# Kernel optimization log

Hardware: AMD Instinct MI355X
Metric: run time of the kernel (lower is better)

The kernel has to match this reference:

```python
import jax, jax.numpy as jnp
import numpy as np

H = 16          # n_heads
HID = 64        # QASS MLP hidden dim


def setup_inputs() -> dict:
    key = jax.random.key(0)
    ks = jax.random.split(key, 12)
    B, N, D = 2, 2048, 1024
    Dh = D // H
    inp = {
        "query": jax.random.normal(ks[0], (B, N, D), jnp.float32),
        "key": jax.random.normal(ks[1], (B, N, D), jnp.float32),
        "value": jax.random.normal(ks[2], (B, N, D), jnp.float32),
        "allowed_mask": jnp.ones((1, 1, N, N), dtype=bool),
        # projection weights, torch Linear convention: y = x @ W.T, W: [out, in]
        "wq": jax.random.normal(ks[3], (D, D), jnp.float32) * (D ** -0.5),
        "wk": jax.random.normal(ks[4], (D, D), jnp.float32) * (D ** -0.5),
        "wv": jax.random.normal(ks[5], (D, D), jnp.float32) * (D ** -0.5),
        "wo": jax.random.normal(ks[6], (D, D), jnp.float32) * (D ** -0.5),
        # QASS scaler weights
        "wb1": jax.random.normal(ks[7], (HID, 1), jnp.float32),          # mlp_base[0]
        "wb2": jax.random.normal(ks[8], (H * Dh, HID), jnp.float32) * (HID ** -0.5),  # mlp_base[2]
        "wg1": jax.random.normal(ks[9], (HID, Dh), jnp.float32) * (Dh ** -0.5),       # mlp_gate[0]
        "wg2": jax.random.normal(ks[10], (Dh, HID), jnp.float32) * (HID ** -0.5),     # mlp_gate[2]
        "n_context": 2048,
    }
    return inp


def _gelu(x):
    return jax.nn.gelu(x, approximate=False)  # torch nn.GELU default (erf)


def reference(query, key, value, allowed_mask, wq, wk, wv, wo, wb1, wb2, wg1, wg2, n_context):
    B, N, D = query.shape
    Dh = D // H

    def split_heads(x):  # [B,N,D] -> [B,H,N,Dh]
        return x.reshape(B, N, H, Dh).transpose(0, 2, 1, 3)

    q = split_heads(query @ wq.T)
    k = split_heads(key @ wk.T)
    v = split_heads(value @ wv.T)

    # QASS scaling: q * base(log n) * (1 + tanh(gate(q)))   (n_context > 1)
    log_n = jnp.log(jnp.asarray(n_context, jnp.float32))
    base = (_gelu(log_n * wb1[:, 0]) @ wb2.T).reshape(1, H, 1, Dh)  # [1,H,1,Dh]
    gate = 1.0 + jnp.tanh(_gelu(q @ wg1.T) @ wg2.T)                  # [B,H,N,Dh]
    q = q * base * gate

    scores = jnp.einsum("bhnd,bhmd->bhnm", q, k) / jnp.sqrt(jnp.float32(Dh))
    scores = jnp.where(allowed_mask, scores, -jnp.inf)
    attn = jax.nn.softmax(scores, axis=-1)  # dropout p=0 -> identity
    out = jnp.einsum("bhnm,bhmd->bhnd", attn, v)
    out = out.transpose(0, 2, 1, 3).reshape(B, N, D)
    return out @ wo.T
```

## Files before the change

### kernel.cpp

```cpp
#include <hip/hip_runtime.h>
#include <math.h>


typedef _Float16 half_t;
using half8   = __attribute__((ext_vector_type(8))) _Float16;
using bhalf8  = __attribute__((ext_vector_type(8))) short;
using floatx4 = __attribute__((ext_vector_type(4))) float;

__device__ inline unsigned short f2bf(float f) {
  union { float f; unsigned int u; } v; v.f = f;
  unsigned int u = v.u;
  u = u + 0x7fffu + ((u >> 16) & 1u);
  return (unsigned short)(u >> 16);
}
__device__ inline float bf2f(unsigned short h) {
  union { unsigned int u; float f; } v; v.u = ((unsigned int)h) << 16;
  return v.f;
}
__device__ inline float gelu_f(float x) {
  return 0.5f * x * (1.0f + erff(x * 0.70710678118654752440f));
}
__device__ __forceinline__ unsigned int cvtpk_bf16(float lo, float hi) {
  unsigned int r;
  asm("v_cvt_pk_bf16_f32 %0, %1, %2" : "=v"(r) : "v"(lo), "v"(hi));
  return r;
}

#define MFMAF16(a, b, c)  __builtin_amdgcn_mfma_f32_16x16x32_f16((a), (b), (c), 0, 0, 0)
#define MFMABF16(a, b, c) __builtin_amdgcn_mfma_f32_16x16x32_bf16((a), (b), (c), 0, 0, 0)

__device__ __forceinline__ void dma16(const void* g, void* l) {
  __builtin_amdgcn_global_load_lds(
      (const __attribute__((address_space(1))) unsigned int*)g,
      (__attribute__((address_space(3))) unsigned int*)l, 16, 0, 0);
}

__global__ __launch_bounds__(256) void k_cvtbase(
    const float* __restrict__ q, const float* __restrict__ k, const float* __restrict__ v,
    const float* __restrict__ wq, const float* __restrict__ wk,
    const float* __restrict__ wv, const float* __restrict__ wo,
    half_t* __restrict__ q16, half_t* __restrict__ k16, half_t* __restrict__ v16,
    half_t* __restrict__ w16,
    const float* __restrict__ wb1, const float* __restrict__ wb2,
    const int* __restrict__ nctx, float* __restrict__ base_out) {
  int tid = threadIdx.x;
  if (blockIdx.x >= 8192) {
    __shared__ float h1[64];
    float logn = logf((float)(*nctx));
    if (tid < 64) h1[tid] = gelu_f(logn * wb1[tid]);
    __syncthreads();
    int i = (blockIdx.x - 8192) * 256 + tid;
    float s = 0.f;
#pragma unroll
    for (int j = 0; j < 64; j++) s += h1[j] * wb2[i * 64 + j];
    base_out[i] = s;
    return;
  }
  size_t e = ((size_t)blockIdx.x * 256 + tid) * 8;
  const float* src; half_t* dst; size_t off;
  if (e < (size_t)3 * 4194304) {
    int t = (int)(e >> 22); off = e & 4194303;
    src = (t == 0) ? q : (t == 1 ? k : v);
    dst = (t == 0) ? q16 : (t == 1 ? k16 : v16);
  } else {
    size_t e2 = e - (size_t)3 * 4194304;
    int t = (int)(e2 >> 20); off = (e2 & 1048575);
    src = (t == 0) ? wq : (t == 1 ? wk : (t == 2 ? wv : wo));
    dst = w16 + (size_t)t * 1048576;
  }
  float4 a = *(const float4*)(src + off);
  float4 b = *(const float4*)(src + off + 4);
  half8 h;
  h[0] = (half_t)a.x; h[1] = (half_t)a.y; h[2] = (half_t)a.z; h[3] = (half_t)a.w;
  h[4] = (half_t)b.x; h[5] = (half_t)b.y; h[6] = (half_t)b.z; h[7] = (half_t)b.w;
  *(half8*)(dst + off) = h;
}

template <int MODE>
__global__ __launch_bounds__(256, 3) void k_gemm(const half_t* __restrict__ Abase,
                                                 const half_t* __restrict__ Wbase,
                                                 half_t* __restrict__ qp16,
                                                 half_t* __restrict__ kswz,
                                                 unsigned short* __restrict__ vtl,
                                                 float* __restrict__ outf) {
  const int z = (MODE == 0) ? blockIdx.z : 0;
  const half_t* Ag = Abase + (size_t)z * 4194304;
  const half_t* Wg = Wbase + (size_t)z * 1048576;
  __shared__ __align__(16) half_t SM[2][128 * 64];
  half_t* As = SM[0];
  half_t* Bs = SM[1];
  const int tid = threadIdx.x, lane = tid & 63, w = tid >> 6;
  const int quad = lane >> 4, lm = lane & 15, a7 = lm & 7;
  const int wm = w >> 1, wn = w & 1;
  const int bm0 = blockIdx.y * 128, bn0 = blockIdx.x * 128;

  const floatx4 zero4 = {0.f, 0.f, 0.f, 0.f};
  floatx4 acc[4][4];
#pragma unroll
  for (int i = 0; i < 4; i++)
#pragma unroll
    for (int j = 0; j < 4; j++) acc[i][j] = zero4;

  for (int kk = 0; kk < 1024; kk += 64) {
    __syncthreads();
#pragma unroll
    for (int i = 0; i < 4; i++) {
      int tr = w * 32 + i * 8 + (lane >> 3);
      int c = (lane & 7) ^ (tr & 7);
      dma16((const char*)Ag + ((size_t)(bm0 + tr) * 1024 + kk + c * 8) * 2,
            (char*)As + (w * 32 + i * 8) * 128);
      dma16((const char*)Wg + ((size_t)(bn0 + tr) * 1024 + kk + c * 8) * 2,
            (char*)Bs + (w * 32 + i * 8) * 128);
    }
    __syncthreads();

#pragma unroll
    for (int kc = 0; kc < 2; kc++) {
      half8 af[4], bf[4];
#pragma unroll
      for (int tm = 0; tm < 4; tm++)
        af[tm] = *(const half8*)&As[(wm * 64 + tm * 16 + lm) * 64
                                    + (((kc * 4 + quad) ^ a7) << 3)];
#pragma unroll
      for (int tn = 0; tn < 4; tn++)
        bf[tn] = *(const half8*)&Bs[(wn * 64 + tn * 16 + lm) * 64
                                    + (((kc * 4 + quad) ^ a7) << 3)];
#pragma unroll
      for (int tm = 0; tm < 4; tm++)
#pragma unroll
        for (int tn = 0; tn < 4; tn++)
          acc[tm][tn] = MFMAF16(af[tm], bf[tn], acc[tm][tn]);
    }
  }

  if constexpr (MODE == 3) {
#pragma unroll
    for (int tm = 0; tm < 4; tm++)
#pragma unroll
      for (int tn = 0; tn < 4; tn++)
#pragma unroll
        for (int rr = 0; rr < 4; rr++) {
          int gm = bm0 + wm * 64 + tm * 16 + quad * 4 + rr;
          int gn = bn0 + wn * 64 + tn * 16 + lm;
          outf[(size_t)gm * 1024 + gn] = acc[tm][tn][rr];
        }
  } else if (z == 0) {
#pragma unroll
    for (int tm = 0; tm < 4; tm++)
#pragma unroll
      for (int tn = 0; tn < 4; tn++)
#pragma unroll
        for (int rr = 0; rr < 4; rr++) {
          int gm = bm0 + wm * 64 + tm * 16 + quad * 4 + rr;
          int gn = bn0 + wn * 64 + tn * 16 + lm;
          int b = gm >> 11, n = gm & 2047, hd = gn >> 6, d = gn & 63;
          qp16[((size_t)((b << 4) + hd) * 2048 + n) * 64 + d] = (half_t)acc[tm][tn][rr];
        }
  } else if (z == 1) {
    half_t* smh = (half_t*)&SM[0][0];
    __syncthreads();
#pragma unroll
    for (int tm = 0; tm < 4; tm++)
#pragma unroll
      for (int tn = 0; tn < 4; tn++) {
        int gnl = wn * 64 + tn * 16 + lm;
        int hl = gnl >> 6, d = gnl & 63;
#pragma unroll
        for (int rr = 0; rr < 4; rr++) {
          int nl = wm * 64 + tm * 16 + quad * 4 + rr;
          int sw = ((((d >> 3) ^ (nl & 7)) << 3) | (d & 7));
          smh[(hl * 128 + nl) * 64 + sw] = (half_t)acc[tm][tn][rr];
        }
      }
    __syncthreads();
    {
      const int b = bm0 >> 11, n0 = bm0 & 2047, hd0 = bn0 >> 6;
#pragma unroll
      for (int c = 0; c < 8; c++) {
        int lin = (c * 256 + tid) * 8;
        int hl = lin >> 13, nl = (lin >> 6) & 127, j0 = lin & 63;
        size_t row = (size_t)((b << 4) + hd0 + hl) * 2048 + n0 + nl;
        *(half8*)(kswz + row * 64 + j0) = *(const half8*)(smh + lin);
      }
    }
  } else {
    unsigned short* sm = (unsigned short*)&SM[0][0];
    __syncthreads();
#pragma unroll
    for (int tm = 0; tm < 4; tm++) {
      int nlb = wm * 64 + tm * 16 + quad * 4;
      int tl = (nlb >> 6) & 1, nnb = nlb & 63;
      int kc4 = nnb >> 5;
      int qd = (nnb >> 2) & 3;
      int j4 = (nnb >> 4) & 1;
#pragma unroll
      for (int tn = 0; tn < 4; tn++) {
        int gnl = wn * 64 + tn * 16 + lm;
        int hl = gnl >> 6, d = gnl & 63;
        int inner0 = (qd * 16 + (d & 15)) * 32 + (d >> 4) * 8 + j4 * 4;
        unsigned int u0 = __float_as_uint(acc[tm][tn][0]) + 0x8000u;
        unsigned int u1 = __float_as_uint(acc[tm][tn][1]) + 0x8000u;
        unsigned int u2 = __float_as_uint(acc[tm][tn][2]) + 0x8000u;
        unsigned int u3 = __float_as_uint(acc[tm][tn][3]) + 0x8000u;
        uint2 pk;
        pk.x = __builtin_amdgcn_perm(u1, u0, 0x07060302u);
        pk.y = __builtin_amdgcn_perm(u3, u2, 0x07060302u);
        *(uint2*)&sm[(((hl * 2 + tl) * 2 + kc4) * 2048) + inner0] = pk;
      }
    }
    __syncthreads();
    {
      const int b = bm0 >> 11, t0 = (bm0 & 2047) >> 6, hd0 = bn0 >> 6;
#pragma unroll
      for (int c = 0; c < 8; c++) {
        int lin = (c * 256 + tid) * 8;
        int page = lin >> 11;
        int hl = page >> 2, tl = (page >> 1) & 1, kc4 = page & 1;
        int inner = lin & 2047;
        size_t idx = ((size_t)(((b << 4) + hd0 + hl) * 32 + t0 + tl) * 2 + kc4) * 2048
                   + (size_t)inner;
        *(bhalf8*)(vtl + idx) = *(const bhalf8*)(sm + lin);
      }
    }
  }
}

__global__ __launch_bounds__(256) void k_gate(const half_t* __restrict__ qp,
                                              const float* __restrict__ base_v,
                                              const float* __restrict__ wg1,
                                              const float* __restrict__ wg2,
                                              half_t* __restrict__ qs) {
  __shared__ __align__(16) half_t W1[64 * 72];
  __shared__ __align__(16) half_t W2[64 * 72];
  __shared__ __align__(16) half_t HT[4][16 * 72];
  const int tid = threadIdx.x, lane = tid & 63, w = tid >> 6;
  const int quad = lane >> 4, lm = lane & 15;
  for (int i = tid; i < 4096; i += 256) {
    int j = i >> 6, d = i & 63;
    W1[j * 72 + d] = (half_t)wg1[i];
    W2[j * 72 + d] = (half_t)wg2[i];
  }
  __syncthreads();
  const int R0 = blockIdx.x * 256;
  const int hd = (R0 >> 11) & 15;
  float bsev[4];
#pragma unroll
  for (int tn = 0; tn < 4; tn++) bsev[tn] = base_v[hd * 64 + tn * 16 + lm];
  const float cs = 0.18033688011112042f;
  const floatx4 zero4 = {0.f, 0.f, 0.f, 0.f};
  half_t* ht = HT[w];

  for (int ti = 0; ti < 4; ti++) {
    int r0 = R0 + w * 64 + ti * 16;
    half8 aq0 = *(const half8*)&qp[(size_t)(r0 + lm) * 64 + quad * 8];
    half8 aq1 = *(const half8*)&qp[(size_t)(r0 + lm) * 64 + 32 + quad * 8];
    floatx4 hc[4];
#pragma unroll
    for (int tn = 0; tn < 4; tn++) {
      half8 b0 = *(const half8*)&W1[(tn * 16 + lm) * 72 + quad * 8];
      half8 b1 = *(const half8*)&W1[(tn * 16 + lm) * 72 + 32 + quad * 8];
      floatx4 t = zero4;
      t = MFMAF16(aq0, b0, t);
      t = MFMAF16(aq1, b1, t);
      hc[tn] = t;
    }
#pragma unroll
    for (int tn = 0; tn < 4; tn++)
#pragma unroll
      for (int rr = 0; rr < 4; rr++)
        ht[(quad * 4 + rr) * 72 + tn * 16 + lm] = (half_t)gelu_f(hc[tn][rr]);
    half8 ah0 = *(const half8*)&ht[lm * 72 + quad * 8];
    half8 ah1 = *(const half8*)&ht[lm * 72 + 32 + quad * 8];
#pragma unroll
    for (int tn = 0; tn < 4; tn++) {
      half8 b0 = *(const half8*)&W2[(tn * 16 + lm) * 72 + quad * 8];
      half8 b1 = *(const half8*)&W2[(tn * 16 + lm) * 72 + 32 + quad * 8];
      floatx4 t = zero4;
      t = MFMAF16(ah0, b0, t);
      t = MFMAF16(ah1, b1, t);
#pragma unroll
      for (int rr = 0; rr < 4; rr++) {
        int row = r0 + quad * 4 + rr;
        int d = tn * 16 + lm;
        float qv = (float)qp[(size_t)row * 64 + d];
        float g = 1.0f + tanhf(t[rr]);
        qs[(size_t)row * 64 + d] = (half_t)(qv * bsev[tn] * g * cs);
      }
    }
  }
}

__global__ __launch_bounds__(256, 2) void k_attn(const half_t* __restrict__ qs,
                                                 const half_t* __restrict__ kswz,
                                                 const unsigned short* __restrict__ vtl,
                                                 unsigned short* __restrict__ Opart,
                                                 float* __restrict__ rpart) {
  __shared__ __align__(16) half_t KH[2][64 * 64];

  const int tid = threadIdx.x;
  const int lane = tid & 63;
  const int w = tid >> 6;
  const int quad = lane >> 4;
  const int lm = lane & 15;
  const int a7 = lm & 7;
  const int hd = blockIdx.x;
  const int qg = blockIdx.y >> 1, half = blockIdx.y & 1;
  const int b = blockIdx.z;
  const int bh = b * 16 + hd;
  const size_t hb = (size_t)bh * 2048 * 64;
  const char* khT = (const char*)(kswz + hb);
  const unsigned short* vtT = vtl + (size_t)bh * 32 * 4096;

  half8 qh[4][2];
#pragma unroll
  for (int rg = 0; rg < 4; rg++)
#pragma unroll
    for (int kc = 0; kc < 2; kc++)
      qh[rg][kc] = *(const half8*)(qs + hb
          + (size_t)(qg * 256 + w * 64 + rg * 16 + lm) * 64 + kc * 32 + quad * 8);

  const floatx4 zero4 = {0.f, 0.f, 0.f, 0.f};
  floatx4 O[4][4];
#pragma unroll
  for (int rg = 0; rg < 4; rg++)
#pragma unroll
    for (int dt = 0; dt < 4; dt++) O[rg][dt] = zero4;
  floatx4 racc[4];
#pragma unroll
  for (int rg = 0; rg < 4; rg++) racc[rg] = zero4;
  const short one_bf = (short)0x3F80;
  const bhalf8 vones = {one_bf, one_bf, one_bf, one_bf,
                        one_bf, one_bf, one_bf, one_bf};

  const int lo16 = lane * 16;
  const size_t g0 = (size_t)half * 16 * 8192;

#pragma unroll
  for (int r = 0; r < 2; r++) {
    int sb = (w * 2 + r) * 1024;
    dma16(khT + g0 + sb + lo16, (char*)KH[0] + sb);
  }

  for (int t = 0; t < 16; t++) {
    const int cur = t & 1;
    __syncthreads();

    const unsigned short* vb = vtT + ((size_t)(half * 16 + t) * 2) * 2048 + lane * 32;
    bhalf8 vf[2][4];
#pragma unroll
    for (int kc4 = 0; kc4 < 2; kc4++)
#pragma unroll
      for (int dt = 0; dt < 4; dt++)
        vf[kc4][dt] = *(const bhalf8*)(vb + kc4 * 2048 + dt * 8);

    if (t < 15) {
      const size_t gof = g0 + (size_t)(t + 1) * 8192;
#pragma unroll
      for (int r = 0; r < 2; r++) {
        int sb = (w * 2 + r) * 1024;
        dma16(khT + gof + sb + lo16, (char*)KH[cur ^ 1] + sb);
      }
    }

    const half_t* kh_ = KH[cur];

#pragma unroll
    for (int p = 0; p < 2; p++) {
      floatx4 s[2][4];
#pragma unroll
      for (int ri = 0; ri < 2; ri++)
#pragma unroll
        for (int kb = 0; kb < 4; kb++) s[ri][kb] = zero4;

      __builtin_amdgcn_s_setprio(1);
#pragma unroll
      for (int kb = 0; kb < 4; kb++)
#pragma unroll
        for (int kc = 0; kc < 2; kc++) {
          int addr = (kb * 16 + lm) * 64 + (((kc * 4 + quad) ^ a7) << 3);
          half8 khf = *(const half8*)&kh_[addr];
#pragma unroll
          for (int ri = 0; ri < 2; ri++)
            s[ri][kb] = MFMAF16(khf, qh[p * 2 + ri][kc], s[ri][kb]);
        }
      __builtin_amdgcn_s_setprio(0);

#pragma unroll
      for (int ri = 0; ri < 2; ri++) {
        const int rg = p * 2 + ri;
        float e[4][4];
#pragma unroll
        for (int kb = 0; kb < 4; kb++)
#pragma unroll
          for (int rr = 0; rr < 4; rr++)
            e[kb][rr] = __builtin_amdgcn_exp2f(s[ri][kb][rr]);

        __builtin_amdgcn_s_setprio(1);
#pragma unroll
        for (int kc4 = 0; kc4 < 2; kc4++) {
          union { unsigned int w4[4]; bhalf8 v; } pa;
          pa.w4[0] = cvtpk_bf16(e[2 * kc4][0],     e[2 * kc4][1]);
          pa.w4[1] = cvtpk_bf16(e[2 * kc4][2],     e[2 * kc4][3]);
          pa.w4[2] = cvtpk_bf16(e[2 * kc4 + 1][0], e[2 * kc4 + 1][1]);
          pa.w4[3] = cvtpk_bf16(e[2 * kc4 + 1][2], e[2 * kc4 + 1][3]);
          racc[rg] = MFMABF16(pa.v, vones, racc[rg]);
#pragma unroll
          for (int dt = 0; dt < 4; dt++)
            O[rg][dt] = MFMABF16(pa.v, vf[kc4][dt], O[rg][dt]);
        }
        __builtin_amdgcn_s_setprio(0);
      }
    }
  }

  unsigned short* op = Opart + (size_t)half * 65536 * 64;
  float* rp = rpart + (size_t)half * 65536;
#pragma unroll
  for (int rg = 0; rg < 4; rg++) {
#pragma unroll
    for (int rr = 0; rr < 4; rr++) {
      int n = qg * 256 + w * 64 + rg * 16 + quad * 4 + rr;
      size_t row = (size_t)bh * 2048 + n;
      if (lm == 0) rp[row] = racc[rg][rr];
#pragma unroll
      for (int dt = 0; dt < 4; dt++)
        op[row * 64 + dt * 16 + lm] = f2bf(O[rg][dt][rr]);
    }
  }
}

__global__ __launch_bounds__(256) void k_combine(const unsigned short* __restrict__ Opart,
                                                 const float* __restrict__ rpart,
                                                 half_t* __restrict__ obf) {
  size_t e = ((size_t)blockIdx.x * 256 + threadIdx.x) * 8;
  size_t row = e >> 6; int d0 = (int)(e & 63);
  float inv = 1.0f / (rpart[row] + rpart[65536 + row]);
  bhalf8 o0 = *(const bhalf8*)&Opart[row * 64 + d0];
  bhalf8 o1 = *(const bhalf8*)&Opart[(size_t)65536 * 64 + row * 64 + d0];
  int b = (int)(row >> 15), h = (int)((row >> 11) & 15), n = (int)(row & 2047);
  half8 o;
#pragma unroll
  for (int j = 0; j < 8; j++)
    o[j] = (half_t)((bf2f((unsigned short)o0[j]) + bf2f((unsigned short)o1[j])) * inv);
  *(half8*)&obf[((size_t)(b * 2048 + n)) * 1024 + h * 64 + d0] = o;
}

extern "C" void kernel_launch(void* const* d_in, const int* in_sizes, int n_in,
                              void* d_out, int out_size, void* d_ws, size_t ws_size,
                              hipStream_t stream) {
  const float* query = (const float*)d_in[0];
  const float* key_  = (const float*)d_in[1];
  const float* value = (const float*)d_in[2];
  const float* wq  = (const float*)d_in[4];
  const float* wk  = (const float*)d_in[5];
  const float* wv  = (const float*)d_in[6];
  const float* wo  = (const float*)d_in[7];
  const float* wb1 = (const float*)d_in[8];
  const float* wb2 = (const float*)d_in[9];
  const float* wg1 = (const float*)d_in[10];
  const float* wg2 = (const float*)d_in[11];
  const int* nctx  = (const int*)d_in[12];
  float* out = (float*)d_out;

  char* ws = (char*)d_ws;
  size_t o = 0;
  float* base_v = (float*)(ws + o); o += 4096;
  half_t* q16   = (half_t*)(ws + o); o += (size_t)4096 * 1024 * 2;
  half_t* k16   = (half_t*)(ws + o); o += (size_t)4096 * 1024 * 2;
  half_t* v16   = (half_t*)(ws + o); o += (size_t)4096 * 1024 * 2;
  half_t* w16   = (half_t*)(ws + o); o += (size_t)4 * 1024 * 1024 * 2;
  half_t* qp16  = (half_t*)(ws + o); o += (size_t)4096 * 1024 * 2;
  half_t* kswz  = (half_t*)(ws + o); o += (size_t)4096 * 1024 * 2;
  unsigned short* vtl = (unsigned short*)(ws + o); o += (size_t)4096 * 1024 * 2;
  unsigned short* Opart = (unsigned short*)(ws + o); o += (size_t)2 * 65536 * 64 * 2;
  float* rpart = (float*)(ws + o); o += (size_t)2 * 65536 * 4;
  half_t* qs  = q16;
  half_t* obf = k16;

  k_cvtbase<<<8196, 256, 0, stream>>>(query, key_, value, wq, wk, wv, wo,
                                      q16, k16, v16, w16, wb1, wb2, nctx, base_v);
  k_gemm<0><<<dim3(8, 32, 3), 256, 0, stream>>>(q16, w16, qp16, kswz, vtl, nullptr);
  k_gate<<<256, 256, 0, stream>>>(qp16, base_v, wg1, wg2, qs);
  k_attn<<<dim3(16, 16, 2), 256, 0, stream>>>(qs, kswz, vtl, Opart, rpart);
  k_combine<<<2048, 256, 0, stream>>>(Opart, rpart, obf);
  k_gemm<3><<<dim3(8, 32, 1), 256, 0, stream>>>(obf, w16 + (size_t)3 * 1048576,
                                                nullptr, nullptr, nullptr, out);
}
```

Baseline: 264.1 us.

## Double-buffer GEMM K-loop with async prefetch of next 32-wide tile

Rewrites the projection GEMM main loop to use two LDS buffers of K=32 each, issuing the direct-to-LDS loads for the next tile before computing on the current one. One barrier per iteration replaces the previous two, so global loads overlap with MFMA work. The swizzle pattern is redesigned for 32-wide rows, and the K step halves, which doubles the loop iteration count and barrier frequency.

```diff
diff --git a/kernel.cpp b/kernel.cpp
--- a/kernel.cpp
+++ b/kernel.cpp
@@ -86,11 +86,9 @@
   const int z = (MODE == 0) ? blockIdx.z : 0;
   const half_t* Ag = Abase + (size_t)z * 4194304;
   const half_t* Wg = Wbase + (size_t)z * 1048576;
-  __shared__ __align__(16) half_t SM[2][128 * 64];
-  half_t* As = SM[0];
-  half_t* Bs = SM[1];
+  __shared__ __align__(16) half_t SM[4][128 * 32];
   const int tid = threadIdx.x, lane = tid & 63, w = tid >> 6;
-  const int quad = lane >> 4, lm = lane & 15, a7 = lm & 7;
+  const int quad = lane >> 4, lm = lane & 15;
   const int wm = w >> 1, wn = w & 1;
   const int bm0 = blockIdx.y * 128, bn0 = blockIdx.x * 128;
 
@@ -101,36 +99,49 @@
 #pragma unroll
     for (int j = 0; j < 4; j++) acc[i][j] = zero4;
 
-  for (int kk = 0; kk < 1024; kk += 64) {
-    __syncthreads();
-#pragma unroll
-    for (int i = 0; i < 4; i++) {
-      int tr = w * 32 + i * 8 + (lane >> 3);
-      int c = (lane & 7) ^ (tr & 7);
-      dma16((const char*)Ag + ((size_t)(bm0 + tr) * 1024 + kk + c * 8) * 2,
-            (char*)As + (w * 32 + i * 8) * 128);
-      dma16((const char*)Wg + ((size_t)(bn0 + tr) * 1024 + kk + c * 8) * 2,
-            (char*)Bs + (w * 32 + i * 8) * 128);
-    }
-    __syncthreads();
-
-#pragma unroll
-    for (int kc = 0; kc < 2; kc++) {
-      half8 af[4], bf[4];
-#pragma unroll
-      for (int tm = 0; tm < 4; tm++)
-        af[tm] = *(const half8*)&As[(wm * 64 + tm * 16 + lm) * 64
-                                    + (((kc * 4 + quad) ^ a7) << 3)];
+  const int j4 = lane >> 2;
+  const int cs = (lane & 3) ^ (((j4 & 3) + (j4 >> 2)) & 3);
+  const int ub = ((lm & 3) + (lm >> 2)) & 3;
+
+#pragma unroll
+  for (int i = 0; i < 2; i++) {
+    int tr = w * 32 + i * 16 + j4;
+    dma16((const char*)Ag + ((size_t)(bm0 + tr) * 1024 + cs * 8) * 2,
+          (char*)SM[0] + (w * 32 + i * 16) * 64);
+    dma16((const char*)Wg + ((size_t)(bn0 + tr) * 1024 + cs * 8) * 2,
+          (char*)SM[2] + (w * 32 + i * 16) * 64);
+  }
+
+  for (int kk = 0; kk < 1024; kk += 32) {
+    const int cur = (kk >> 5) & 1;
+    __syncthreads();
+    if (kk < 992) {
+#pragma unroll
+      for (int i = 0; i < 2; i++) {
+        int tr = w * 32 + i * 16 + j4;
+        dma16((const char*)Ag + ((size_t)(bm0 + tr) * 1024 + kk + 32 + cs * 8) * 2,
+              (char*)SM[cur ^ 1] + (w * 32 + i * 16) * 64);
+        dma16((const char*)Wg + ((size_t)(bn0 + tr) * 1024 + kk + 32 + cs * 8) * 2,
+              (char*)SM[2 + (cur ^ 1)] + (w * 32 + i * 16) * 64);
+      }
+    }
+
+    const half_t* as_ = SM[cur];
+    const half_t* bs_ = SM[2 + cur];
+    half8 af[4], bf[4];
+#pragma unroll
+    for (int tm = 0; tm < 4; tm++)
+      af[tm] = *(const half8*)&as_[(wm * 64 + tm * 16 + lm) * 32
+                                   + ((quad ^ ub) << 3)];
+#pragma unroll
+    for (int tn = 0; tn < 4; tn++)
+      bf[tn] = *(const half8*)&bs_[(wn * 64 + tn * 16 + lm) * 32
+                                   + ((quad ^ ub) << 3)];
+#pragma unroll
+    for (int tm = 0; tm < 4; tm++)
 #pragma unroll
       for (int tn = 0; tn < 4; tn++)
-        bf[tn] = *(const half8*)&Bs[(wn * 64 + tn * 16 + lm) * 64
-                                    + (((kc * 4 + quad) ^ a7) << 3)];
-#pragma unroll
-      for (int tm = 0; tm < 4; tm++)
-#pragma unroll
-        for (int tn = 0; tn < 4; tn++)
-          acc[tm][tn] = MFMAF16(af[tm], bf[tn], acc[tm][tn]);
-    }
+        acc[tm][tn] = MFMAF16(af[tm], bf[tn], acc[tm][tn]);
   }
 
   if constexpr (MODE == 3) {
@@ -192,12 +203,12 @@
       int tl = (nlb >> 6) & 1, nnb = nlb & 63;
       int kc4 = nnb >> 5;
       int qd = (nnb >> 2) & 3;
-      int j4 = (nnb >> 4) & 1;
+      int jb = (nnb >> 4) & 1;
 #pragma unroll
       for (int tn = 0; tn < 4; tn++) {
         int gnl = wn * 64 + tn * 16 + lm;
         int hl = gnl >> 6, d = gnl & 63;
-        int inner0 = (qd * 16 + (d & 15)) * 32 + (d >> 4) * 8 + j4 * 4;
+        int inner0 = (qd * 16 + (d & 15)) * 32 + (d >> 4) * 8 + jb * 4;
         unsigned int u0 = __float_as_uint(acc[tm][tn][0]) + 0x8000u;
         unsigned int u1 = __float_as_uint(acc[tm][tn][1]) + 0x8000u;
         unsigned int u2 = __float_as_uint(acc[tm][tn][2]) + 0x8000u;
```

After: 250.5 us (median of 2 runs). 5.2% less time.
